# Kernel optimization log

Measured on AMD Instinct MI355X. Metric: run time of the kernel, lower is better.

## Reference

```python
import jax, jax.numpy as jnp
import numpy as np

B, S, D, H = 2, 2048, 1024, 16
HD = D // H  # 64


def setup_inputs() -> dict:
    key = jax.random.key(0)
    ks = jax.random.split(key, 6)
    x = jax.random.normal(ks[0], (B, S, D), dtype=jnp.float32)
    # rotary frequencies: theta = 10000^{-2i/hd}, angles = pos * theta
    inv_freq = 1.0 / (10000.0 ** (jnp.arange(0, HD, 2, dtype=jnp.float32) / HD))  # [HD/2]
    angles = jnp.arange(S, dtype=jnp.float32)[:, None] * inv_freq[None, :]  # [S, HD/2]
    freqs_cos = jnp.cos(angles)
    freqs_sin = jnp.sin(angles)
    scale = 0.02
    w_qkv = jax.random.normal(ks[1], (3 * D, D), dtype=jnp.float32) * scale
    b_qkv = jnp.zeros((3 * D,), dtype=jnp.float32)
    w_dense = jax.random.normal(ks[2], (D, D), dtype=jnp.float32) * scale
    b_dense = jnp.zeros((D,), dtype=jnp.float32)
    return {"x": x, "w_qkv": w_qkv, "b_qkv": b_qkv, "w_dense": w_dense,
            "b_dense": b_dense, "freqs_cos": freqs_cos, "freqs_sin": freqs_sin}


def _apply_rope(t, cos, sin):
    # t: [B, S, H, HD]; cos/sin: [S, HD/2] broadcast as [1, S, 1, HD/2]
    tr = t.reshape(t.shape[:-1] + (HD // 2, 2))
    x0, x1 = tr[..., 0], tr[..., 1]
    c = cos[None, :, None, :]
    s = sin[None, :, None, :]
    o0 = x0 * c - x1 * s  # real part of complex multiply
    o1 = x0 * s + x1 * c  # imag part
    return jnp.stack([o0, o1], axis=-1).reshape(t.shape)


def reference(x, w_qkv, b_qkv, w_dense, b_dense, freqs_cos, freqs_sin):
    b, s, d = x.shape
    qkv = x @ w_qkv.T + b_qkv              # [B, S, 3D]
    qkv = qkv.reshape(b, s, 3, H, HD)
    q, k, v = qkv[:, :, 0], qkv[:, :, 1], qkv[:, :, 2]  # [B, S, H, HD]
    q = _apply_rope(q, freqs_cos, freqs_sin)
    k = _apply_rope(k, freqs_cos, freqs_sin)
    # causal SDPA, scale = 1/sqrt(head_dim)
    q = q.transpose(0, 2, 1, 3)  # [B, H, S, HD]
    k = k.transpose(0, 2, 1, 3)
    v = v.transpose(0, 2, 1, 3)
    scores = jnp.einsum('bhqd,bhkd->bhqk', q, k) / jnp.sqrt(jnp.float32(HD))
    causal = jnp.tril(jnp.ones((s, s), dtype=bool))
    scores = jnp.where(causal[None, None], scores, jnp.finfo(scores.dtype).min)
    attn = jax.nn.softmax(scores, axis=-1)
    ctx = jnp.einsum('bhqk,bhkd->bhqd', attn, v)   # [B, H, S, HD]
    ctx = ctx.transpose(0, 2, 1, 3).reshape(b, s, d)
    return ctx @ w_dense.T + b_dense
```

## Files before the change

### kernel.cpp

```cpp
#include <hip/hip_runtime.h>
#include <stdint.h>

#define Bb 2
#define Ss 2048
#define Dd 1024
#define Hh 16
#define HDd 64

typedef float f32x4 __attribute__((ext_vector_type(4)));
typedef __bf16 bf16x8 __attribute__((ext_vector_type(8)));
typedef __bf16 bf16x2 __attribute__((ext_vector_type(2)));
typedef short s16x8 __attribute__((ext_vector_type(8)));

__device__ inline unsigned short f2bf(float f) {
  unsigned u = __builtin_bit_cast(unsigned, f);
  u += 0x7fffu + ((u >> 16) & 1u);
  return (unsigned short)(u >> 16);
}
__device__ inline float bf2f(unsigned short h) {
  unsigned u = ((unsigned)h) << 16;
  return __builtin_bit_cast(float, u);
}
__device__ inline unsigned pkcvt(float a, float b) {
  bf16x2 v;
  v[0] = (__bf16)a;
  v[1] = (__bf16)b;
  return __builtin_bit_cast(unsigned, v);
}
__device__ inline float ex2(float x) {
#if __has_builtin(__builtin_amdgcn_exp2f)
  return __builtin_amdgcn_exp2f(x);
#else
  float r;
  asm("v_exp_f32 %0, %1\n\ts_nop 1" : "=v"(r) : "v"(x));
  return r;
#endif
}
__device__ inline int swz(int row, int soff) {
  return (row << 6) + ((((soff >> 3) ^ (row & 7)) << 3) | (soff & 7));
}

#define GLDS(dst, src)                                                        \
  __builtin_amdgcn_global_load_lds(                                           \
      (const __attribute__((address_space(1))) void*)(src),                   \
      (__attribute__((address_space(3))) void*)(dst), 16, 0, 0)

__global__ void cast_all(const float* __restrict__ x, const float* __restrict__ wq,
                         const float* __restrict__ wd, unsigned short* __restrict__ dst) {
  int i = blockIdx.x * blockDim.x + threadIdx.x;
  float4 v;
  if (i < 1048576) v = ((const float4*)x)[i];
  else if (i < 1835008) v = ((const float4*)wq)[i - 1048576];
  else v = ((const float4*)wd)[i - 1835008];
  ushort4 o;
  o.x = f2bf(v.x); o.y = f2bf(v.y); o.z = f2bf(v.z); o.w = f2bf(v.w);
  ((ushort4*)dst)[i] = o;
}

__global__ __launch_bounds__(512, 2) void gemm_qkv(
    const unsigned short* __restrict__ A, const unsigned short* __restrict__ Bw,
    const float* __restrict__ bias, unsigned short* __restrict__ qkvout,
    unsigned short* __restrict__ vtout,
    const float* __restrict__ fc, const float* __restrict__ fs) {
  const int K = 1024, NT = 16;
  __shared__ __align__(16) unsigned short Ah[2][2][128 * 32];
  __shared__ __align__(16) unsigned short Bh[2][2][192 * 32];
  const int tid = threadIdx.x;
  const int w = tid >> 6, l = tid & 63;
  const int lg = l >> 4, lr = l & 15;
  const int wm = w >> 2, wn = w & 3;
  int id = blockIdx.y * gridDim.x + blockIdx.x;
  const int nwg = gridDim.x * gridDim.y;
  id = (id & 7) * (nwg >> 3) + (id >> 3);
  const int bx = id % gridDim.x, by = id / gridDim.x;
  const int mbase = by * 128, nbase = bx * 192;

  const unsigned short *as0, *bs0, *bs1, *bs2;
  {
    int r_ = tid >> 2, s_ = (tid & 3) ^ ((r_ >> 1) & 3);
    as0 = A + (size_t)(mbase + r_) * K + s_ * 8;
    bs0 = Bw + (size_t)(nbase + r_) * K + s_ * 8;
    int cb2 = 512 + tid;
    int h2 = cb2 >= 768;
    int cw2 = cb2 - h2 * 768;
    int r2 = cw2 >> 2, s2 = (cw2 & 3) ^ ((r2 >> 1) & 3);
    bs1 = Bw + (size_t)(nbase + r2) * K + h2 * 32 + s2 * 8;
    int cw3 = 256 + tid;
    int r3 = cw3 >> 2, s3 = (cw3 & 3) ^ ((r3 >> 1) & 3);
    bs2 = Bw + (size_t)(nbase + r3) * K + 32 + s3 * 8;
  }
#define STAGE(buf, k0)                                                        \
  GLDS(&Ah[buf][0][0] + tid * 8, as0 + (k0));                                 \
  GLDS(&Ah[buf][0][0] + 4096 + tid * 8, as0 + 32 + (k0));                     \
  GLDS(&Bh[buf][0][0] + tid * 8, bs0 + (k0));                                 \
  GLDS(&Bh[buf][0][0] + (512 + tid) * 8, bs1 + (k0));                         \
  GLDS(&Bh[buf][0][0] + (1024 + tid) * 8, bs2 + (k0));

  STAGE(0, 0);
  __syncthreads();

  f32x4 acc[4][3] = {};
  for (int t = 0; t < NT; ++t) {
    const int cur = t & 1;
    if (t + 1 < NT) { STAGE(cur ^ 1, (t + 1) * 64); }
#pragma unroll
    for (int h = 0; h < 2; ++h) {
      bf16x8 bfr[3], af[4];
#pragma unroll
      for (int ni = 0; ni < 3; ++ni) {
        int row = wn * 48 + ni * 16 + lr;
        bfr[ni] = *(const bf16x8*)(&Bh[cur][h][row * 32 + ((lg ^ ((row >> 1) & 3)) << 3)]);
      }
#pragma unroll
      for (int j = 0; j < 4; ++j) {
        int row = wm * 64 + j * 16 + lr;
        af[j] = *(const bf16x8*)(&Ah[cur][h][row * 32 + ((lg ^ ((row >> 1) & 3)) << 3)]);
      }
      __builtin_amdgcn_s_setprio(1);
#pragma unroll
      for (int j = 0; j < 4; ++j)
#pragma unroll
        for (int ni = 0; ni < 3; ++ni)
          acc[j][ni] = __builtin_amdgcn_mfma_f32_16x16x32_bf16(
              af[j], bfr[ni], acc[j][ni], 0, 0, 0);
      __builtin_amdgcn_s_setprio(0);
    }
    __syncthreads();
  }
#undef STAGE

#pragma unroll
  for (int mi = 0; mi < 4; ++mi)
#pragma unroll
    for (int ni = 0; ni < 3; ++ni) {
      int col = nbase + wn * 48 + ni * 16 + lr;
      float bi = bias[col];
      int row0 = mbase + wm * 64 + mi * 16 + lg * 4;
      float o4[4];
#pragma unroll
      for (int r = 0; r < 4; ++r) o4[r] = acc[mi][ni][r] + bi;
      int sect = col >> 10;
      int d = col & 63;
      int srow0 = row0 & 2047;
      if (sect < 2) {
        int p = d >> 1;
#pragma unroll
        for (int r = 0; r < 4; ++r) {
          float vp = __shfl_xor(o4[r], 1);
          float c = fc[(srow0 + r) * 32 + p];
          float s = fs[(srow0 + r) * 32 + p];
          float o = (d & 1) ? (vp * s + o4[r] * c) : (o4[r] * c - vp * s);
          qkvout[(size_t)(row0 + r) * 3072 + col] = f2bf(o);
        }
      } else {
        int bh = (row0 >> 11) * 16 + ((col >> 6) & 15);
        uint2 o;
        o.x = pkcvt(o4[0], o4[1]);
        o.y = pkcvt(o4[2], o4[3]);
        *(uint2*)&vtout[((size_t)(bh * 64 + d)) * 2048 + srow0] = o;
      }
    }
}

__global__ __launch_bounds__(256, 2) void gemm_out(
    const unsigned short* __restrict__ A, const unsigned short* __restrict__ Bw,
    const float* __restrict__ bias, float* __restrict__ Cout) {
  const int M = 4096, N = 1024, K = 1024;
  __shared__ __align__(16) unsigned short As[64 * 32];
  __shared__ __align__(16) unsigned short Bs[128 * 32];
  const int tid = threadIdx.x;
  const int w = tid >> 6, l = tid & 63;
  const int lg = l >> 4, lr = l & 15;
  const int wm = w >> 1, wn = w & 1;
  int id = blockIdx.y * gridDim.x + blockIdx.x;
  const int nwg = gridDim.x * gridDim.y;
  id = (id & 7) * (nwg >> 3) + (id >> 3);
  const int bx = id % gridDim.x, by = id / gridDim.x;
  const int mbase = by * 64, nbase = bx * 128;

  const unsigned short *as0, *bs0, *bs1;
  {
    int r_ = tid >> 2, s_ = (tid & 3) ^ ((r_ >> 1) & 3);
    as0 = A + (size_t)(mbase + r_) * K + s_ * 8;
    bs0 = Bw + (size_t)(nbase + r_) * K + s_ * 8;
    int r2 = 64 + r_, s2 = (tid & 3) ^ ((r2 >> 1) & 3);
    bs1 = Bw + (size_t)(nbase + r2) * K + s2 * 8;
  }

  f32x4 acc[2][4] = {};
  for (int k0 = 0; k0 < K; k0 += 32) {
    GLDS(As + tid * 8, as0 + k0);
    GLDS(Bs + tid * 8, bs0 + k0);
    GLDS(Bs + (256 + tid) * 8, bs1 + k0);
    __syncthreads();
    bf16x8 af[2], bfr[4];
#pragma unroll
    for (int mi = 0; mi < 2; ++mi) {
      int row = wm * 32 + mi * 16 + lr;
      af[mi] = *(const bf16x8*)(As + row * 32 + ((lg ^ ((row >> 1) & 3)) << 3));
    }
#pragma unroll
    for (int ni = 0; ni < 4; ++ni) {
      int row = wn * 64 + ni * 16 + lr;
      bfr[ni] = *(const bf16x8*)(Bs + row * 32 + ((lg ^ ((row >> 1) & 3)) << 3));
    }
    __builtin_amdgcn_s_setprio(1);
#pragma unroll
    for (int mi = 0; mi < 2; ++mi)
#pragma unroll
      for (int ni = 0; ni < 4; ++ni)
        acc[mi][ni] = __builtin_amdgcn_mfma_f32_16x16x32_bf16(
            af[mi], bfr[ni], acc[mi][ni], 0, 0, 0);
    __builtin_amdgcn_s_setprio(0);
    __syncthreads();
  }

#pragma unroll
  for (int mi = 0; mi < 2; ++mi) {
#pragma unroll
    for (int ni = 0; ni < 4; ++ni) {
      int col = nbase + wn * 64 + ni * 16 + lr;
      float bi = bias[col];
#pragma unroll
      for (int r = 0; r < 4; ++r) {
        int row = mbase + wm * 32 + mi * 16 + lg * 4 + r;
        Cout[(size_t)row * N + col] = acc[mi][ni][r] + bi;
      }
    }
  }
}

__global__ __launch_bounds__(256, 3) void attn(
    const unsigned short* __restrict__ qkv, const unsigned short* __restrict__ vt,
    unsigned short* __restrict__ ctx) {
  __shared__ __align__(16) unsigned short Ks[2][64 * 64];
  __shared__ __align__(16) unsigned short Vs[2][64 * 64];
  __shared__ __align__(16) unsigned short Ps[4][32 * 64];
  int did = blockIdx.x;
  int x = did & 7, rest = did >> 3;
  int bh = x * 4 + (rest & 3);
  int qi = 31 - (rest >> 2);
  int b = bh >> 4, h = bh & 15;
  int qbase = qi * 64;
  int tid = threadIdx.x;
  int w = tid >> 6, l = tid & 63;
  int lg = l >> 4, lr = l & 15;
  int wq = w & 1, wk = w >> 1;
  int qw = wq * 32;

  bf16x8 qb[2][2];
#pragma unroll
  for (int mi = 0; mi < 2; ++mi)
#pragma unroll
    for (int kc = 0; kc < 2; ++kc) {
      s16x8 qr = *(const s16x8*)(qkv +
          (size_t)(b * Ss + qbase + qw + mi * 16 + lr) * 3072 + h * 64 + kc * 32 + lg * 8);
      bf16x8 qs;
#pragma unroll
      for (int e = 0; e < 8; ++e)
        qs[e] = (__bf16)(bf2f((unsigned short)qr[e]) * 0.18033688f);
      qb[mi][kc] = qs;
    }

  int c1 = tid, c2 = 256 + tid;
  int r1 = c1 >> 3, s1 = ((c1 & 7) ^ (r1 & 7)) * 8;
  int r2 = c2 >> 3, s2 = ((c2 & 7) ^ (r2 & 7)) * 8;
  const unsigned short* kg1 = qkv + ((size_t)(b * Ss) + r1) * 3072 + 1024 + h * 64 + s1;
  const unsigned short* kg2 = qkv + ((size_t)(b * Ss) + r2) * 3072 + 1024 + h * 64 + s2;
  const unsigned short* vg1 = vt + ((size_t)bh * 64 + r1) * 2048 + s1;
  const unsigned short* vg2 = vt + ((size_t)bh * 64 + r2) * 2048 + s2;
#define STAGEKV(kt)                                                           \
  {                                                                           \
    int tt_ = (kt) & 1;                                                       \
    GLDS(&Ks[tt_][0] + c1 * 8, kg1 + (size_t)(kt) * 64 * 3072);               \
    GLDS(&Ks[tt_][0] + c2 * 8, kg2 + (size_t)(kt) * 64 * 3072);               \
    GLDS(&Vs[tt_][0] + c1 * 8, vg1 + (kt) * 64);                              \
    GLDS(&Vs[tt_][0] + c2 * 8, vg2 + (kt) * 64);                              \
  }

  int nkt = qi + 1;
  int nsup = (nkt + 1) >> 1;

  STAGEKV(0);
  if (1 < nkt) STAGEKV(1);
  __syncthreads();

  f32x4 acc[4][2] = {};
  float mrow[2] = {-1e30f, -1e30f}, lsum[2] = {0.f, 0.f};

  for (int j = 0; j < nsup; ++j) {
    int kt = 2 * j + wk;
    if (kt < nkt) {
      f32x4 st[4][2] = {};
      __builtin_amdgcn_s_setprio(1);
#pragma unroll
      for (int kc = 0; kc < 2; ++kc) {
#pragma unroll
        for (int ni = 0; ni < 4; ++ni) {
          bf16x8 ka = *(const bf16x8*)&Ks[wk][swz(ni * 16 + lr, kc * 32 + lg * 8)];
#pragma unroll
          for (int mi = 0; mi < 2; ++mi)
            st[ni][mi] = __builtin_amdgcn_mfma_f32_16x16x32_bf16(
                ka, qb[mi][kc], st[ni][mi], 0, 0, 0);
        }
      }
      __builtin_amdgcn_s_setprio(0);

      float tm[2] = {-1e30f, -1e30f};
      if (kt == qi) {
#pragma unroll
        for (int mi = 0; mi < 2; ++mi) {
          int rq = qw + mi * 16 + lr;
#pragma unroll
          for (int ni = 0; ni < 4; ++ni)
#pragma unroll
            for (int r4 = 0; r4 < 4; ++r4) {
              float s = st[ni][mi][r4];
              if (ni * 16 + lg * 4 + r4 > rq) s = -1e30f;
              st[ni][mi][r4] = s;
              tm[mi] = fmaxf(tm[mi], s);
            }
        }
      } else {
#pragma unroll
        for (int mi = 0; mi < 2; ++mi)
#pragma unroll
          for (int ni = 0; ni < 4; ++ni)
#pragma unroll
            for (int r4 = 0; r4 < 4; ++r4) tm[mi] = fmaxf(tm[mi], st[ni][mi][r4]);
      }
      bool ok = (tm[0] <= mrow[0] + 8.0f) && (tm[1] <= mrow[1] + 8.0f);
      if (!__all(ok)) {
#pragma unroll
        for (int mi = 0; mi < 2; ++mi) {
          float t = fmaxf(tm[mi], __shfl_xor(tm[mi], 16));
          t = fmaxf(t, __shfl_xor(t, 32));
          float mnew = fmaxf(mrow[mi], t);
          float alpha = ex2(mrow[mi] - mnew);
          lsum[mi] *= alpha;
#pragma unroll
          for (int nd = 0; nd < 4; ++nd)
#pragma unroll
            for (int r4 = 0; r4 < 4; ++r4) acc[nd][mi][r4] *= alpha;
          mrow[mi] = mnew;
        }
      }
#pragma unroll
      for (int mi = 0; mi < 2; ++mi) {
        float sum = 0.f;
#pragma unroll
        for (int ni = 0; ni < 4; ++ni)
#pragma unroll
          for (int r4 = 0; r4 < 4; ++r4) {
            float pe = ex2(st[ni][mi][r4] - mrow[mi]);
            st[ni][mi][r4] = pe;
            sum += pe;
          }
        lsum[mi] += sum;
#pragma unroll
        for (int ni = 0; ni < 4; ++ni) {
          uint2 wv;
          wv.x = pkcvt(st[ni][mi][0], st[ni][mi][1]);
          wv.y = pkcvt(st[ni][mi][2], st[ni][mi][3]);
          *(uint2*)&Ps[w][swz(mi * 16 + lr, ni * 16 + lg * 4)] = wv;
        }
      }
      __builtin_amdgcn_s_setprio(1);
#pragma unroll
      for (int kc = 0; kc < 2; ++kc) {
        bf16x8 pbf[2];
#pragma unroll
        for (int mi = 0; mi < 2; ++mi)
          pbf[mi] = *(const bf16x8*)&Ps[w][swz(mi * 16 + lr, kc * 32 + lg * 8)];
#pragma unroll
        for (int nd = 0; nd < 4; ++nd) {
          bf16x8 va = *(const bf16x8*)&Vs[wk][swz(nd * 16 + lr, kc * 32 + lg * 8)];
#pragma unroll
          for (int mi = 0; mi < 2; ++mi)
            acc[nd][mi] = __builtin_amdgcn_mfma_f32_16x16x32_bf16(
                va, pbf[mi], acc[nd][mi], 0, 0, 0);
        }
      }
      __builtin_amdgcn_s_setprio(0);
    }

    if (j + 1 < nsup) {
      __syncthreads();
      int t0 = 2 * (j + 1), t1 = t0 + 1;
      STAGEKV(t0);
      if (t1 < nkt) STAGEKV(t1);
      __syncthreads();
    }
  }
#undef STAGEKV

#pragma unroll
  for (int mi = 0; mi < 2; ++mi) {
    lsum[mi] += __shfl_xor(lsum[mi], 16);
    lsum[mi] += __shfl_xor(lsum[mi], 32);
  }
  __syncthreads();
  float* aS0 = (float*)Ks;
  float* aS1 = (float*)Vs;
  float* mlS = (float*)Ps;
  if (wk == 1) {
    int base = (wq * 64 + l) * 16;
#pragma unroll
    for (int nd = 0; nd < 4; ++nd) {
      *(f32x4*)(aS0 + base + nd * 4) = acc[nd][0];
      *(f32x4*)(aS1 + base + nd * 4) = acc[nd][1];
    }
    int mb = (wq * 64 + l) * 4;
    mlS[mb] = mrow[0]; mlS[mb + 1] = lsum[0];
    mlS[mb + 2] = mrow[1]; mlS[mb + 3] = lsum[1];
  }
  __syncthreads();
  if (wk == 0) {
    int base = (wq * 64 + l) * 16;
    int mb = (wq * 64 + l) * 4;
#pragma unroll
    for (int mi = 0; mi < 2; ++mi) {
      const float* as = (mi ? aS1 : aS0) + base;
      float m1 = mlS[mb + mi * 2], l1 = mlS[mb + mi * 2 + 1];
      float M = fmaxf(mrow[mi], m1);
      float s0 = ex2(mrow[mi] - M), s1 = ex2(m1 - M);
      float inv = 1.0f / (lsum[mi] * s0 + l1 * s1);
      float f0 = s0 * inv, f1 = s1 * inv;
      int qg = qbase + qw + mi * 16 + lr;
#pragma unroll
      for (int nd = 0; nd < 4; ++nd) {
        f32x4 a1 = *(const f32x4*)(as + nd * 4);
        uint2 o;
        o.x = pkcvt(acc[nd][mi][0] * f0 + a1[0] * f1,
                    acc[nd][mi][1] * f0 + a1[1] * f1);
        o.y = pkcvt(acc[nd][mi][2] * f0 + a1[2] * f1,
                    acc[nd][mi][3] * f0 + a1[3] * f1);
        *(uint2*)&ctx[((size_t)(b * Ss) + qg) * 1024 + h * 64 + nd * 16 + lg * 4] = o;
      }
    }
  }
}

extern "C" void kernel_launch(void* const* d_in, const int* in_sizes, int n_in,
                              void* d_out, int out_size, void* d_ws, size_t ws_size,
                              hipStream_t stream) {
  const float* x       = (const float*)d_in[0];
  const float* w_qkv   = (const float*)d_in[1];
  const float* b_qkv   = (const float*)d_in[2];
  const float* w_dense = (const float*)d_in[3];
  const float* b_dense = (const float*)d_in[4];
  const float* fc      = (const float*)d_in[5];
  const float* fs      = (const float*)d_in[6];
  float* out = (float*)d_out;

  char* ws = (char*)d_ws;
  unsigned short* xb    = (unsigned short*)(ws);
  unsigned short* wqkvb = (unsigned short*)(ws + (8ull  << 20));
  unsigned short* wdb   = (unsigned short*)(ws + (14ull << 20));
  unsigned short* qkvb  = (unsigned short*)(ws + (16ull << 20));
  unsigned short* vt    = (unsigned short*)(ws + (40ull << 20));

  cast_all<<<8192, 256, 0, stream>>>(x, w_qkv, w_dense, xb);

  gemm_qkv<<<dim3(16, 32), 512, 0, stream>>>(xb, wqkvb, b_qkv, qkvb, vt, fc, fs);
  attn<<<1024, 256, 0, stream>>>(qkvb, vt, xb );
  gemm_out<<<dim3(8, 64), 256, 0, stream>>>(xb, wdb, b_dense, out);
}
```

Measured before the change: 96.62 us.

## Load V tiles directly from global into registers instead of LDS staging

The attention kernel no longer stages V tiles through shared memory. Each wave now loads its V fragments straight from the transposed V buffer into registers, issuing the loads after the QK MFMAs so their latency can overlap with the softmax. This drops the V shared buffers and cuts LDS traffic and footprint. The cost is duplicate global/L2 reads of V, since the two query-half waves for a given key tile fetch the same data, plus extra register pressure. The epilogue reduction scratch is remapped onto the two halves of the K buffer.

New measurement: 108.4 us. 1.12x slower.

```diff
diff --git a/kernel.cpp b/kernel.cpp
--- a/kernel.cpp
+++ b/kernel.cpp
@@ -234,7 +234,6 @@
     const unsigned short* __restrict__ qkv, const unsigned short* __restrict__ vt,
     unsigned short* __restrict__ ctx) {
   __shared__ __align__(16) unsigned short Ks[2][64 * 64];
-  __shared__ __align__(16) unsigned short Vs[2][64 * 64];
   __shared__ __align__(16) unsigned short Ps[4][32 * 64];
   int did = blockIdx.x;
   int x = did & 7, rest = did >> 3;
@@ -267,22 +266,19 @@
   int r2 = c2 >> 3, s2 = ((c2 & 7) ^ (r2 & 7)) * 8;
   const unsigned short* kg1 = qkv + ((size_t)(b * Ss) + r1) * 3072 + 1024 + h * 64 + s1;
   const unsigned short* kg2 = qkv + ((size_t)(b * Ss) + r2) * 3072 + 1024 + h * 64 + s2;
-  const unsigned short* vg1 = vt + ((size_t)bh * 64 + r1) * 2048 + s1;
-  const unsigned short* vg2 = vt + ((size_t)bh * 64 + r2) * 2048 + s2;
-#define STAGEKV(kt)                                                           \
+  const unsigned short* vtb = vt + (size_t)bh * 64 * 2048;
+#define STAGEK(kt)                                                            \
   {                                                                           \
     int tt_ = (kt) & 1;                                                       \
     GLDS(&Ks[tt_][0] + c1 * 8, kg1 + (size_t)(kt) * 64 * 3072);               \
     GLDS(&Ks[tt_][0] + c2 * 8, kg2 + (size_t)(kt) * 64 * 3072);               \
-    GLDS(&Vs[tt_][0] + c1 * 8, vg1 + (kt) * 64);                              \
-    GLDS(&Vs[tt_][0] + c2 * 8, vg2 + (kt) * 64);                              \
   }
 
   int nkt = qi + 1;
   int nsup = (nkt + 1) >> 1;
 
-  STAGEKV(0);
-  if (1 < nkt) STAGEKV(1);
+  STAGEK(0);
+  if (1 < nkt) STAGEK(1);
   __syncthreads();
 
   f32x4 acc[4][2] = {};
@@ -305,6 +301,13 @@
         }
       }
       __builtin_amdgcn_s_setprio(0);
+      bf16x8 va[2][4];
+#pragma unroll
+      for (int kc = 0; kc < 2; ++kc)
+#pragma unroll
+        for (int nd = 0; nd < 4; ++nd)
+          va[kc][nd] = *(const bf16x8*)&vtb[(size_t)(nd * 16 + lr) * 2048 +
+                                            kt * 64 + kc * 32 + lg * 8];
 
       float tm[2] = {-1e30f, -1e30f};
       if (kt == qi) {
@@ -374,11 +377,10 @@
           pbf[mi] = *(const bf16x8*)&Ps[w][swz(mi * 16 + lr, kc * 32 + lg * 8)];
 #pragma unroll
         for (int nd = 0; nd < 4; ++nd) {
-          bf16x8 va = *(const bf16x8*)&Vs[wk][swz(nd * 16 + lr, kc * 32 + lg * 8)];
 #pragma unroll
           for (int mi = 0; mi < 2; ++mi)
             acc[nd][mi] = __builtin_amdgcn_mfma_f32_16x16x32_bf16(
-                va, pbf[mi], acc[nd][mi], 0, 0, 0);
+                va[kc][nd], pbf[mi], acc[nd][mi], 0, 0, 0);
         }
       }
       __builtin_amdgcn_s_setprio(0);
@@ -387,12 +389,12 @@
     if (j + 1 < nsup) {
       __syncthreads();
       int t0 = 2 * (j + 1), t1 = t0 + 1;
-      STAGEKV(t0);
-      if (t1 < nkt) STAGEKV(t1);
+      STAGEK(t0);
+      if (t1 < nkt) STAGEK(t1);
       __syncthreads();
     }
   }
-#undef STAGEKV
+#undef STAGEK
 
 #pragma unroll
   for (int mi = 0; mi < 2; ++mi) {
@@ -400,9 +402,9 @@
     lsum[mi] += __shfl_xor(lsum[mi], 32);
   }
   __syncthreads();
-  float* aS0 = (float*)Ks;
-  float* aS1 = (float*)Vs;
-  float* mlS = (float*)Ps;
+  float* aS0 = (float*)&Ks[0][0];
+  float* aS1 = (float*)&Ks[1][0];
+  float* mlS = (float*)&Ps[0][0];
   if (wk == 1) {
     int base = (wq * 64 + l) * 16;
 #pragma unroll
```
